# Kernel tuning notes

Measured on AMD Instinct MI355X. Metric: run time of the kernel, lower is better.

## Reference

```python
import jax, jax.numpy as jnp
import numpy as np

NUM_HEADS = 16
D_MODEL = 1024
DEPTH = D_MODEL // NUM_HEADS
B, S = 4, 1024  # q,k seq len = S; v seq len = S-1


def setup_inputs() -> dict:
    key = jax.random.key(0)
    ks = jax.random.split(key, 6)
    scale = 1.0 / np.sqrt(D_MODEL)
    return {
        "v": jax.random.normal(ks[0], (B, S - 1, D_MODEL), dtype=jnp.float32),
        "k": jax.random.normal(ks[1], (B, S, D_MODEL), dtype=jnp.float32),
        "q": jax.random.normal(ks[2], (B, S, D_MODEL), dtype=jnp.float32),
        "mask": jnp.zeros((B, S - 1, S - 1), dtype=jnp.float32),
        "Wv": jax.random.normal(ks[3], (D_MODEL, D_MODEL), dtype=jnp.float32) * scale,
        "bv": jnp.zeros((D_MODEL,), dtype=jnp.float32),
        "Wd": jax.random.normal(ks[4], (D_MODEL, D_MODEL), dtype=jnp.float32) * scale,
        "bd": jnp.zeros((D_MODEL,), dtype=jnp.float32),
    }


def _split_heads(x):
    # (B, T, d_model) -> (B, H, T, depth)
    b, t, _ = x.shape
    return x.reshape(b, t, NUM_HEADS, DEPTH).transpose(0, 2, 1, 3)


def reference(v, k, q, mask, Wv, bv, Wd, bd):
    # 3-D q/k path: qq=q, kk=k (q_layers/k_layers/wq/wk unused)
    vv = v @ Wv + bv                       # (B, S-1, d_model)
    qh = _split_heads(q)                   # (B, H, S, depth)
    kh = _split_heads(k)                   # (B, H, S, depth)
    vh = _split_heads(vv)                  # (B, H, S-1, depth)

    scores = jnp.einsum('bhqd,bhkd->bhqk', qh, kh)      # (B, H, S, S)
    scores = scores[:, :, 1:, :-1]                      # (B, H, S-1, S-1)
    dk = jnp.asarray(DEPTH, scores.dtype)
    nl = jax.nn.relu(scores / jnp.sqrt(dk))
    nl = nl + mask[:, None, :, :] * (-1e9)
    att = jax.nn.softmax(nl, axis=-1)                   # (B, H, S-1, S-1)

    out = jnp.einsum('bhqk,bhkd->bhqd', att, vh)        # (B, H, S-1, depth)
    out = out.transpose(0, 2, 1, 3).reshape(v.shape[0], -1, D_MODEL)  # (B, S-1, d_model)
    output = out @ Wd + bd
    return output, att
```

## Files before the change

### kernel.cpp

```cpp
#include <hip/hip_runtime.h>
#include <hip/hip_bf16.h>

#define NUM_HEADS 16
#define DM 1024
#define DEPTH 64
#define BB 4
#define SS 1024
#define SL 1023
#define M_ROWS (BB*SL)

typedef __attribute__((ext_vector_type(8))) short short8;
typedef __attribute__((ext_vector_type(4))) float floatx4;

__device__ inline unsigned short f2bf(float f) {
  __hip_bfloat16 hb = __float2bfloat16(f);
  return *reinterpret_cast<unsigned short*>(&hb);
}
__device__ inline short8 ld_frag(const unsigned short* p) {
  return *reinterpret_cast<const short8*>(p);
}

template <bool A_BF16, bool OUT_BF16>
__global__ __launch_bounds__(256) void gemm_bias(
    const void* __restrict__ Av, const float* __restrict__ B,
    const float* __restrict__ bias, void* __restrict__ Cv, int M)
{
  __shared__ unsigned short bshT[128][40];
  const int tid = threadIdx.x;
  const int w = tid >> 6, lane = tid & 63, q4 = lane >> 4, l16 = lane & 15;
  const int wm = w >> 1, wn = w & 1;
  const int rb = blockIdx.y * 128 + wm * 64;
  const int cb = blockIdx.x * 128;
  const int wc = wn * 64;

  floatx4 acc[4][4];
  #pragma unroll
  for (int i = 0; i < 4; i++)
    #pragma unroll
    for (int j = 0; j < 4; j++) acc[i][j] = (floatx4){0.f,0.f,0.f,0.f};

  const int sn = tid & 127;
  const int sk = (tid >> 7) * 16;

  for (int k0 = 0; k0 < DM; k0 += 32) {
    __syncthreads();
    {
      const float* bp = B + (size_t)(k0 + sk) * DM + cb + sn;
      unsigned short tmp[16];
      #pragma unroll
      for (int j = 0; j < 16; j++) tmp[j] = f2bf(bp[(size_t)j * DM]);
      *(uint4*)&bshT[sn][sk]     = *(uint4*)&tmp[0];
      *(uint4*)&bshT[sn][sk + 8] = *(uint4*)&tmp[8];
    }
    __syncthreads();

    short8 af[4];
    #pragma unroll
    for (int i = 0; i < 4; i++) {
      int m = rb + i * 16 + l16;
      if (m < M) {
        if (A_BF16) {
          af[i] = ld_frag((const unsigned short*)Av + (size_t)m * DM + k0 + q4 * 8);
        } else {
          const float* ap = (const float*)Av + (size_t)m * DM + k0 + q4 * 8;
          float4 f0 = *(const float4*)ap;
          float4 f1 = *(const float4*)(ap + 4);
          short8 t;
          t[0]=f2bf(f0.x); t[1]=f2bf(f0.y); t[2]=f2bf(f0.z); t[3]=f2bf(f0.w);
          t[4]=f2bf(f1.x); t[5]=f2bf(f1.y); t[6]=f2bf(f1.z); t[7]=f2bf(f1.w);
          af[i] = t;
        }
      } else {
        af[i] = (short8){0,0,0,0,0,0,0,0};
      }
    }
    #pragma unroll
    for (int jn = 0; jn < 4; jn++) {
      short8 bf = ld_frag(&bshT[wc + jn * 16 + l16][q4 * 8]);
      #pragma unroll
      for (int i = 0; i < 4; i++)
        acc[i][jn] = __builtin_amdgcn_mfma_f32_16x16x32_bf16(af[i], bf, acc[i][jn], 0, 0, 0);
    }
  }

  #pragma unroll
  for (int jn = 0; jn < 4; jn++) {
    int col = cb + wc + jn * 16 + l16;
    float bb = bias[col];
    #pragma unroll
    for (int i = 0; i < 4; i++) {
      #pragma unroll
      for (int r = 0; r < 4; r++) {
        int m = rb + i * 16 + q4 * 4 + r;
        if (m < M) {
          float val = acc[i][jn][r] + bb;
          if (OUT_BF16) ((unsigned short*)Cv)[(size_t)m * DM + col] = f2bf(val);
          else          ((float*)Cv)[(size_t)m * DM + col] = val;
        }
      }
    }
  }
}

__global__ __launch_bounds__(256) void attn_kernel(
    const float* __restrict__ Q, const float* __restrict__ Kg,
    const float* __restrict__ Mask, const unsigned short* __restrict__ VV,
    float* __restrict__ Att, unsigned short* __restrict__ Out2)
{
  const int qt = blockIdx.x, h = blockIdx.y, b = blockIdx.z;
  const int tid = threadIdx.x;
  const int w = tid >> 6, lane = tid & 63, q4 = lane >> 4, l16 = lane & 15;
  const int qi0 = qt * 64;
  const int qb = w * 16;

  __shared__ unsigned short qsh[64][72];
  __shared__ unsigned short ksh[64][72];
  __shared__ unsigned short vshT[64][72];
  __shared__ unsigned short psh[4][16][72];

  {
    int qr = tid >> 2, d0 = (tid & 3) * 16;
    int qi = qi0 + qr;
    unsigned short tmp[16];
    if (qi < SL) {
      const float* src = Q + ((size_t)b * SS + qi + 1) * DM + h * DEPTH + d0;
      #pragma unroll
      for (int j = 0; j < 16; j += 4) {
        float4 f = *(const float4*)(src + j);
        tmp[j+0]=f2bf(f.x); tmp[j+1]=f2bf(f.y); tmp[j+2]=f2bf(f.z); tmp[j+3]=f2bf(f.w);
      }
    } else {
      #pragma unroll
      for (int j = 0; j < 16; j++) tmp[j] = 0;
    }
    *(uint4*)&qsh[qr][d0]     = *(uint4*)&tmp[0];
    *(uint4*)&qsh[qr][d0 + 8] = *(uint4*)&tmp[8];
  }

  auto stageK = [&](int kt) {
    int kr = tid >> 2, d0 = (tid & 3) * 16;
    int kj = kt * 64 + kr;
    unsigned short tmp[16];
    if (kj < SL) {
      const float* src = Kg + ((size_t)b * SS + kj) * DM + h * DEPTH + d0;
      #pragma unroll
      for (int j = 0; j < 16; j += 4) {
        float4 f = *(const float4*)(src + j);
        tmp[j+0]=f2bf(f.x); tmp[j+1]=f2bf(f.y); tmp[j+2]=f2bf(f.z); tmp[j+3]=f2bf(f.w);
      }
    } else {
      #pragma unroll
      for (int j = 0; j < 16; j++) tmp[j] = 0;
    }
    *(uint4*)&ksh[kr][d0]     = *(uint4*)&tmp[0];
    *(uint4*)&ksh[kr][d0 + 8] = *(uint4*)&tmp[8];
  };

  auto stageV = [&](int kt) {
    int d = tid & 63, k16 = (tid >> 6) * 16;
    unsigned short tmp[16];
    #pragma unroll
    for (int j = 0; j < 16; j++) {
      int kj = kt * 64 + k16 + j;
      tmp[j] = (kj < SL) ? VV[((size_t)b * SL + kj) * DM + h * DEPTH + d] : (unsigned short)0;
    }
    *(uint4*)&vshT[d][k16]     = *(uint4*)&tmp[0];
    *(uint4*)&vshT[d][k16 + 8] = *(uint4*)&tmp[8];
  };

  __syncthreads();

  float rsv[4] = {0.f, 0.f, 0.f, 0.f};
  for (int kt = 0; kt < 16; kt++) {
    __syncthreads();
    stageK(kt);
    __syncthreads();
    #pragma unroll
    for (int nt = 0; nt < 4; nt++) {
      floatx4 s = (floatx4){0.f,0.f,0.f,0.f};
      s = __builtin_amdgcn_mfma_f32_16x16x32_bf16(
            ld_frag(&qsh[qb + l16][q4*8]), ld_frag(&ksh[nt*16 + l16][q4*8]), s, 0,0,0);
      s = __builtin_amdgcn_mfma_f32_16x16x32_bf16(
            ld_frag(&qsh[qb + l16][32 + q4*8]), ld_frag(&ksh[nt*16 + l16][32 + q4*8]), s, 0,0,0);
      int kj = kt * 64 + nt * 16 + l16;
      bool kv = kj < SL;
      int qi_b = qi0 + qb + q4 * 4;
      const float* mp = Mask + ((size_t)b * SL + qi_b) * SL + kj;
      #pragma unroll
      for (int r = 0; r < 4; r++) {
        int qi = qi_b + r;
        float mval = (kv && qi < SL) ? mp[(size_t)r * SL] : 0.f;
        float sv = fmaxf(s[r] * 0.125f, 0.f) + mval * (-1e9f);
        float p = kv ? __expf(sv) : 0.f;
        rsv[r] += p;
      }
    }
  }
  #pragma unroll
  for (int r = 0; r < 4; r++) {
    #pragma unroll
    for (int off = 1; off < 16; off <<= 1) rsv[r] += __shfl_xor(rsv[r], off, 64);
  }
  float inv[4];
  #pragma unroll
  for (int r = 0; r < 4; r++) inv[r] = 1.f / rsv[r];

  floatx4 oacc[4];
  #pragma unroll
  for (int i = 0; i < 4; i++) oacc[i] = (floatx4){0.f,0.f,0.f,0.f};

  for (int kt = 0; kt < 16; kt++) {
    __syncthreads();
    stageK(kt);
    stageV(kt);
    __syncthreads();
    #pragma unroll
    for (int nt = 0; nt < 4; nt++) {
      floatx4 s = (floatx4){0.f,0.f,0.f,0.f};
      s = __builtin_amdgcn_mfma_f32_16x16x32_bf16(
            ld_frag(&qsh[qb + l16][q4*8]), ld_frag(&ksh[nt*16 + l16][q4*8]), s, 0,0,0);
      s = __builtin_amdgcn_mfma_f32_16x16x32_bf16(
            ld_frag(&qsh[qb + l16][32 + q4*8]), ld_frag(&ksh[nt*16 + l16][32 + q4*8]), s, 0,0,0);
      int kj = kt * 64 + nt * 16 + l16;
      bool kv = kj < SL;
      int qi_b = qi0 + qb + q4 * 4;
      const float* mp = Mask + ((size_t)b * SL + qi_b) * SL + kj;
      #pragma unroll
      for (int r = 0; r < 4; r++) {
        int qi = qi_b + r;
        bool qv = qi < SL;
        float mval = (kv && qv) ? mp[(size_t)r * SL] : 0.f;
        float sv = fmaxf(s[r] * 0.125f, 0.f) + mval * (-1e9f);
        float p = kv ? __expf(sv) : 0.f;
        float pn = p * inv[r];
        if (kv && qv)
          Att[(((size_t)(b * NUM_HEADS + h)) * SL + qi) * SL + kj] = pn;
        psh[w][q4 * 4 + r][nt * 16 + l16] = f2bf(pn);
      }
    }
    short8 pa0 = ld_frag(&psh[w][l16][q4 * 8]);
    short8 pa1 = ld_frag(&psh[w][l16][32 + q4 * 8]);
    #pragma unroll
    for (int nt2 = 0; nt2 < 4; nt2++) {
      oacc[nt2] = __builtin_amdgcn_mfma_f32_16x16x32_bf16(
                    pa0, ld_frag(&vshT[nt2*16 + l16][q4*8]), oacc[nt2], 0,0,0);
      oacc[nt2] = __builtin_amdgcn_mfma_f32_16x16x32_bf16(
                    pa1, ld_frag(&vshT[nt2*16 + l16][32 + q4*8]), oacc[nt2], 0,0,0);
    }
  }

  #pragma unroll
  for (int nt2 = 0; nt2 < 4; nt2++) {
    #pragma unroll
    for (int r = 0; r < 4; r++) {
      int qi = qi0 + qb + q4 * 4 + r;
      if (qi < SL)
        Out2[((size_t)b * SL + qi) * DM + h * DEPTH + nt2 * 16 + l16] = f2bf(oacc[nt2][r]);
    }
  }
}

extern "C" void kernel_launch(void* const* d_in, const int* in_sizes, int n_in,
                              void* d_out, int out_size, void* d_ws, size_t ws_size,
                              hipStream_t stream) {
  const float* v    = (const float*)d_in[0];
  const float* k    = (const float*)d_in[1];
  const float* q    = (const float*)d_in[2];
  const float* mask = (const float*)d_in[3];
  const float* Wv   = (const float*)d_in[4];
  const float* bv   = (const float*)d_in[5];
  const float* Wd   = (const float*)d_in[6];
  const float* bd   = (const float*)d_in[7];

  float* out = (float*)d_out;
  float* att = out + (size_t)M_ROWS * DM;
  unsigned short* vv   = (unsigned short*)d_ws;
  unsigned short* out2 = vv + (size_t)M_ROWS * DM;

  gemm_bias<false, true><<<dim3(DM/128, (M_ROWS+127)/128), 256, 0, stream>>>(
      (const void*)v, Wv, bv, (void*)vv, M_ROWS);
  attn_kernel<<<dim3(16, NUM_HEADS, BB), 256, 0, stream>>>(q, k, mask, vv, att, out2);
  gemm_bias<true, false><<<dim3(DM/128, (M_ROWS+127)/128), 256, 0, stream>>>(
      (const void*)out2, Wd, bd, (void*)out, M_ROWS);
}
```

Before: 778.4 us.

## Cache unnormalized probabilities in LDS and pre-transpose weights to bf16

The attention kernel now computes QK^T once per block instead of twice. It keeps the unnormalized bf16 probabilities for the full key row in a large LDS buffer, writes the normalized attention rows with coalesced stores, and applies the normalization to the PV output at the end. A new prep kernel converts both weight matrices to bf16 and transposes them, so the GEMMs stage A and B tiles into LDS with vector loads instead of strided per-element fp32 loads. The roughly 132KB of LDS per attention block limits occupancy, and the row sums are now taken from bf16-rounded values.

```diff
diff --git a/kernel.cpp b/kernel.cpp
--- a/kernel.cpp
+++ b/kernel.cpp
@@ -8,6 +8,7 @@
 #define SS 1024
 #define SL 1023
 #define M_ROWS (BB*SL)
+#define M_PAD 4096
 
 typedef __attribute__((ext_vector_type(8))) short short8;
 typedef __attribute__((ext_vector_type(4))) float floatx4;
@@ -16,22 +17,49 @@
   __hip_bfloat16 hb = __float2bfloat16(f);
   return *reinterpret_cast<unsigned short*>(&hb);
 }
+__device__ inline float bf2fu(unsigned short u) {
+  union { unsigned int i; float f; } x; x.i = ((unsigned int)u) << 16; return x.f;
+}
 __device__ inline short8 ld_frag(const unsigned short* p) {
   return *reinterpret_cast<const short8*>(p);
 }
 
-template <bool A_BF16, bool OUT_BF16>
+__global__ __launch_bounds__(256) void prep_wt(
+    const float* __restrict__ Wv, const float* __restrict__ Wd,
+    unsigned short* __restrict__ WvT, unsigned short* __restrict__ WdT)
+{
+  const float* W = blockIdx.z ? Wd : Wv;
+  unsigned short* WT = blockIdx.z ? WdT : WvT;
+  __shared__ unsigned short tile[64][66];
+  int n0 = blockIdx.x * 64, k0 = blockIdx.y * 64;
+  int c = threadIdx.x & 63, g = threadIdx.x >> 6;
+  #pragma unroll
+  for (int i = 0; i < 16; i++) {
+    int kk = g * 16 + i;
+    tile[kk][c] = f2bf(W[(size_t)(k0 + kk) * DM + n0 + c]);
+  }
+  __syncthreads();
+  #pragma unroll
+  for (int i = 0; i < 16; i++) {
+    int nn = g * 16 + i;
+    WT[(size_t)(n0 + nn) * DM + k0 + c] = tile[c][nn];
+  }
+}
+
+template <bool A_FP32, bool OUT_BF16>
 __global__ __launch_bounds__(256) void gemm_bias(
-    const void* __restrict__ Av, const float* __restrict__ B,
+    const void* __restrict__ Av, const unsigned short* __restrict__ BT,
     const float* __restrict__ bias, void* __restrict__ Cv, int M)
 {
-  __shared__ unsigned short bshT[128][40];
+  __shared__ unsigned short Ash[128][32];
+  __shared__ unsigned short Bsh[128][32];
   const int tid = threadIdx.x;
   const int w = tid >> 6, lane = tid & 63, q4 = lane >> 4, l16 = lane & 15;
   const int wm = w >> 1, wn = w & 1;
-  const int rb = blockIdx.y * 128 + wm * 64;
+  const int rb = blockIdx.y * 128;
   const int cb = blockIdx.x * 128;
-  const int wc = wn * 64;
+  const int r0 = tid >> 2;
+  const int kc0 = (tid & 3) * 8;
 
   floatx4 acc[4][4];
   #pragma unroll
@@ -39,61 +67,53 @@
     #pragma unroll
     for (int j = 0; j < 4; j++) acc[i][j] = (floatx4){0.f,0.f,0.f,0.f};
 
-  const int sn = tid & 127;
-  const int sk = (tid >> 7) * 16;
+  const int ra0 = min(rb + r0, M - 1);
+  const int ra1 = min(rb + 64 + r0, M - 1);
 
   for (int k0 = 0; k0 < DM; k0 += 32) {
     __syncthreads();
-    {
-      const float* bp = B + (size_t)(k0 + sk) * DM + cb + sn;
-      unsigned short tmp[16];
-      #pragma unroll
-      for (int j = 0; j < 16; j++) tmp[j] = f2bf(bp[(size_t)j * DM]);
-      *(uint4*)&bshT[sn][sk]     = *(uint4*)&tmp[0];
-      *(uint4*)&bshT[sn][sk + 8] = *(uint4*)&tmp[8];
-    }
-    __syncthreads();
-
-    short8 af[4];
+    if (A_FP32) {
+      const float* g0 = (const float*)Av + (size_t)ra0 * DM + k0 + kc0;
+      const float* g1 = (const float*)Av + (size_t)ra1 * DM + k0 + kc0;
+      float4 x0 = *(const float4*)g0, x1 = *(const float4*)(g0 + 4);
+      float4 y0 = *(const float4*)g1, y1 = *(const float4*)(g1 + 4);
+      unsigned short t0[8] = {f2bf(x0.x),f2bf(x0.y),f2bf(x0.z),f2bf(x0.w),
+                              f2bf(x1.x),f2bf(x1.y),f2bf(x1.z),f2bf(x1.w)};
+      unsigned short t1[8] = {f2bf(y0.x),f2bf(y0.y),f2bf(y0.z),f2bf(y0.w),
+                              f2bf(y1.x),f2bf(y1.y),f2bf(y1.z),f2bf(y1.w)};
+      *(uint4*)&Ash[r0][kc0]      = *(uint4*)t0;
+      *(uint4*)&Ash[64 + r0][kc0] = *(uint4*)t1;
+    } else {
+      *(uint4*)&Ash[r0][kc0]      = *(const uint4*)((const unsigned short*)Av + (size_t)ra0 * DM + k0 + kc0);
+      *(uint4*)&Ash[64 + r0][kc0] = *(const uint4*)((const unsigned short*)Av + (size_t)ra1 * DM + k0 + kc0);
+    }
+    *(uint4*)&Bsh[r0][kc0]      = *(const uint4*)(BT + (size_t)(cb + r0) * DM + k0 + kc0);
+    *(uint4*)&Bsh[64 + r0][kc0] = *(const uint4*)(BT + (size_t)(cb + 64 + r0) * DM + k0 + kc0);
+    __syncthreads();
+
+    short8 af[4], bfr[4];
+    #pragma unroll
+    for (int i = 0; i < 4; i++) af[i]  = ld_frag(&Ash[wm*64 + i*16 + l16][q4*8]);
+    #pragma unroll
+    for (int j = 0; j < 4; j++) bfr[j] = ld_frag(&Bsh[wn*64 + j*16 + l16][q4*8]);
+    #pragma unroll
+    for (int j = 0; j < 4; j++)
+      #pragma unroll
+      for (int i = 0; i < 4; i++)
+        acc[i][j] = __builtin_amdgcn_mfma_f32_16x16x32_bf16(af[i], bfr[j], acc[i][j], 0, 0, 0);
+  }
+
+  #pragma unroll
+  for (int j = 0; j < 4; j++) {
+    int col = cb + wn*64 + j*16 + l16;
+    float bb = bias[col];
     #pragma unroll
     for (int i = 0; i < 4; i++) {
-      int m = rb + i * 16 + l16;
-      if (m < M) {
-        if (A_BF16) {
-          af[i] = ld_frag((const unsigned short*)Av + (size_t)m * DM + k0 + q4 * 8);
-        } else {
-          const float* ap = (const float*)Av + (size_t)m * DM + k0 + q4 * 8;
-          float4 f0 = *(const float4*)ap;
-          float4 f1 = *(const float4*)(ap + 4);
-          short8 t;
-          t[0]=f2bf(f0.x); t[1]=f2bf(f0.y); t[2]=f2bf(f0.z); t[3]=f2bf(f0.w);
-          t[4]=f2bf(f1.x); t[5]=f2bf(f1.y); t[6]=f2bf(f1.z); t[7]=f2bf(f1.w);
-          af[i] = t;
-        }
-      } else {
-        af[i] = (short8){0,0,0,0,0,0,0,0};
-      }
-    }
-    #pragma unroll
-    for (int jn = 0; jn < 4; jn++) {
-      short8 bf = ld_frag(&bshT[wc + jn * 16 + l16][q4 * 8]);
-      #pragma unroll
-      for (int i = 0; i < 4; i++)
-        acc[i][jn] = __builtin_amdgcn_mfma_f32_16x16x32_bf16(af[i], bf, acc[i][jn], 0, 0, 0);
-    }
-  }
-
-  #pragma unroll
-  for (int jn = 0; jn < 4; jn++) {
-    int col = cb + wc + jn * 16 + l16;
-    float bb = bias[col];
-    #pragma unroll
-    for (int i = 0; i < 4; i++) {
       #pragma unroll
       for (int r = 0; r < 4; r++) {
-        int m = rb + i * 16 + q4 * 4 + r;
+        int m = rb + wm*64 + i*16 + q4*4 + r;
         if (m < M) {
-          float val = acc[i][jn][r] + bb;
+          float val = acc[i][j][r] + bb;
           if (OUT_BF16) ((unsigned short*)Cv)[(size_t)m * DM + col] = f2bf(val);
           else          ((float*)Cv)[(size_t)m * DM + col] = val;
         }
@@ -113,10 +133,9 @@
   const int qi0 = qt * 64;
   const int qb = w * 16;
 
+  __shared__ unsigned short psh[64][1032];
   __shared__ unsigned short qsh[64][72];
-  __shared__ unsigned short ksh[64][72];
-  __shared__ unsigned short vshT[64][72];
-  __shared__ unsigned short psh[4][16][72];
+  __shared__ unsigned short kvsh[64][72];
 
   {
     int qr = tid >> 2, d0 = (tid & 3) * 16;
@@ -127,7 +146,7 @@
       #pragma unroll
       for (int j = 0; j < 16; j += 4) {
         float4 f = *(const float4*)(src + j);
-        tmp[j+0]=f2bf(f.x); tmp[j+1]=f2bf(f.y); tmp[j+2]=f2bf(f.z); tmp[j+3]=f2bf(f.w);
+        tmp[j]=f2bf(f.x); tmp[j+1]=f2bf(f.y); tmp[j+2]=f2bf(f.z); tmp[j+3]=f2bf(f.w);
       }
     } else {
       #pragma unroll
@@ -136,116 +155,101 @@
     *(uint4*)&qsh[qr][d0]     = *(uint4*)&tmp[0];
     *(uint4*)&qsh[qr][d0 + 8] = *(uint4*)&tmp[8];
   }
-
-  auto stageK = [&](int kt) {
-    int kr = tid >> 2, d0 = (tid & 3) * 16;
-    int kj = kt * 64 + kr;
-    unsigned short tmp[16];
-    if (kj < SL) {
-      const float* src = Kg + ((size_t)b * SS + kj) * DM + h * DEPTH + d0;
-      #pragma unroll
-      for (int j = 0; j < 16; j += 4) {
-        float4 f = *(const float4*)(src + j);
-        tmp[j+0]=f2bf(f.x); tmp[j+1]=f2bf(f.y); tmp[j+2]=f2bf(f.z); tmp[j+3]=f2bf(f.w);
-      }
-    } else {
-      #pragma unroll
-      for (int j = 0; j < 16; j++) tmp[j] = 0;
-    }
-    *(uint4*)&ksh[kr][d0]     = *(uint4*)&tmp[0];
-    *(uint4*)&ksh[kr][d0 + 8] = *(uint4*)&tmp[8];
-  };
-
-  auto stageV = [&](int kt) {
-    int d = tid & 63, k16 = (tid >> 6) * 16;
-    unsigned short tmp[16];
-    #pragma unroll
-    for (int j = 0; j < 16; j++) {
-      int kj = kt * 64 + k16 + j;
-      tmp[j] = (kj < SL) ? VV[((size_t)b * SL + kj) * DM + h * DEPTH + d] : (unsigned short)0;
-    }
-    *(uint4*)&vshT[d][k16]     = *(uint4*)&tmp[0];
-    *(uint4*)&vshT[d][k16 + 8] = *(uint4*)&tmp[8];
-  };
-
   __syncthreads();
+  const short8 qf0 = ld_frag(&qsh[qb + l16][q4*8]);
+  const short8 qf1 = ld_frag(&qsh[qb + l16][32 + q4*8]);
 
   float rsv[4] = {0.f, 0.f, 0.f, 0.f};
+
   for (int kt = 0; kt < 16; kt++) {
     __syncthreads();
-    stageK(kt);
-    __syncthreads();
+    {
+      int kr = tid >> 2, d0 = (tid & 3) * 16;
+      int kj = kt * 64 + kr;
+      unsigned short tmp[16];
+      if (kj < SL) {
+        const float* src = Kg + ((size_t)b * SS + kj) * DM + h * DEPTH + d0;
+        #pragma unroll
+        for (int j = 0; j < 16; j += 4) {
+          float4 f = *(const float4*)(src + j);
+          tmp[j]=f2bf(f.x); tmp[j+1]=f2bf(f.y); tmp[j+2]=f2bf(f.z); tmp[j+3]=f2bf(f.w);
+        }
+      } else {
+        #pragma unroll
+        for (int j = 0; j < 16; j++) tmp[j] = 0;
+      }
+      *(uint4*)&kvsh[kr][d0]     = *(uint4*)&tmp[0];
+      *(uint4*)&kvsh[kr][d0 + 8] = *(uint4*)&tmp[8];
+    }
+    __syncthreads();
+
     #pragma unroll
     for (int nt = 0; nt < 4; nt++) {
       floatx4 s = (floatx4){0.f,0.f,0.f,0.f};
-      s = __builtin_amdgcn_mfma_f32_16x16x32_bf16(
-            ld_frag(&qsh[qb + l16][q4*8]), ld_frag(&ksh[nt*16 + l16][q4*8]), s, 0,0,0);
-      s = __builtin_amdgcn_mfma_f32_16x16x32_bf16(
-            ld_frag(&qsh[qb + l16][32 + q4*8]), ld_frag(&ksh[nt*16 + l16][32 + q4*8]), s, 0,0,0);
+      s = __builtin_amdgcn_mfma_f32_16x16x32_bf16(qf0, ld_frag(&kvsh[nt*16 + l16][q4*8]), s, 0,0,0);
+      s = __builtin_amdgcn_mfma_f32_16x16x32_bf16(qf1, ld_frag(&kvsh[nt*16 + l16][32 + q4*8]), s, 0,0,0);
       int kj = kt * 64 + nt * 16 + l16;
       bool kv = kj < SL;
       int qi_b = qi0 + qb + q4 * 4;
       const float* mp = Mask + ((size_t)b * SL + qi_b) * SL + kj;
       #pragma unroll
       for (int r = 0; r < 4; r++) {
-        int qi = qi_b + r;
-        float mval = (kv && qi < SL) ? mp[(size_t)r * SL] : 0.f;
-        float sv = fmaxf(s[r] * 0.125f, 0.f) + mval * (-1e9f);
-        float p = kv ? __expf(sv) : 0.f;
-        rsv[r] += p;
-      }
-    }
-  }
-  #pragma unroll
-  for (int r = 0; r < 4; r++) {
-    #pragma unroll
-    for (int off = 1; off < 16; off <<= 1) rsv[r] += __shfl_xor(rsv[r], off, 64);
-  }
-  float inv[4];
-  #pragma unroll
-  for (int r = 0; r < 4; r++) inv[r] = 1.f / rsv[r];
-
-  floatx4 oacc[4];
-  #pragma unroll
-  for (int i = 0; i < 4; i++) oacc[i] = (floatx4){0.f,0.f,0.f,0.f};
-
-  for (int kt = 0; kt < 16; kt++) {
-    __syncthreads();
-    stageK(kt);
-    stageV(kt);
-    __syncthreads();
-    #pragma unroll
-    for (int nt = 0; nt < 4; nt++) {
-      floatx4 s = (floatx4){0.f,0.f,0.f,0.f};
-      s = __builtin_amdgcn_mfma_f32_16x16x32_bf16(
-            ld_frag(&qsh[qb + l16][q4*8]), ld_frag(&ksh[nt*16 + l16][q4*8]), s, 0,0,0);
-      s = __builtin_amdgcn_mfma_f32_16x16x32_bf16(
-            ld_frag(&qsh[qb + l16][32 + q4*8]), ld_frag(&ksh[nt*16 + l16][32 + q4*8]), s, 0,0,0);
-      int kj = kt * 64 + nt * 16 + l16;
-      bool kv = kj < SL;
-      int qi_b = qi0 + qb + q4 * 4;
-      const float* mp = Mask + ((size_t)b * SL + qi_b) * SL + kj;
-      #pragma unroll
-      for (int r = 0; r < 4; r++) {
-        int qi = qi_b + r;
-        bool qv = qi < SL;
+        bool qv = (qi_b + r) < SL;
         float mval = (kv && qv) ? mp[(size_t)r * SL] : 0.f;
         float sv = fmaxf(s[r] * 0.125f, 0.f) + mval * (-1e9f);
         float p = kv ? __expf(sv) : 0.f;
-        float pn = p * inv[r];
-        if (kv && qv)
-          Att[(((size_t)(b * NUM_HEADS + h)) * SL + qi) * SL + kj] = pn;
-        psh[w][q4 * 4 + r][nt * 16 + l16] = f2bf(pn);
-      }
-    }
-    short8 pa0 = ld_frag(&psh[w][l16][q4 * 8]);
-    short8 pa1 = ld_frag(&psh[w][l16][32 + q4 * 8]);
+        unsigned short u = f2bf(p);
+        psh[qb + q4*4 + r][kt*64 + nt*16 + l16] = u;
+        rsv[r] += bf2fu(u);
+      }
+    }
+  }
+
+  float inv4[4];
+  #pragma unroll
+  for (int r = 0; r < 4; r++) {
+    float s = rsv[r];
+    s += __shfl_xor(s, 1, 64); s += __shfl_xor(s, 2, 64);
+    s += __shfl_xor(s, 4, 64); s += __shfl_xor(s, 8, 64);
+    inv4[r] = 1.f / s;
+  }
+
+  #pragma unroll
+  for (int rr = 0; rr < 16; rr++) {
+    int row = qb + rr;
+    int qi = qi0 + row;
+    if (qi < SL) {
+      float iv = __shfl(inv4[rr & 3], (rr >> 2) * 16, 64);
+      float* arow = Att + (((size_t)(b * NUM_HEADS + h)) * SL + qi) * SL;
+      for (int col = lane; col < SL; col += 64)
+        arow[col] = bf2fu(psh[row][col]) * iv;
+    }
+  }
+
+  floatx4 oacc[4];
+  #pragma unroll
+  for (int i = 0; i < 4; i++) oacc[i] = (floatx4){0.f,0.f,0.f,0.f};
+
+  for (int kt = 0; kt < 16; kt++) {
+    __syncthreads();
+    {
+      int d = tid & 63, k16 = (tid >> 6) * 16;
+      unsigned short tmp[16];
+      #pragma unroll
+      for (int j = 0; j < 16; j++) {
+        int kj = kt * 64 + k16 + j;
+        tmp[j] = (kj < SL) ? VV[((size_t)b * SL + kj) * DM + h * DEPTH + d] : (unsigned short)0;
+      }
+      *(uint4*)&kvsh[d][k16]     = *(uint4*)&tmp[0];
+      *(uint4*)&kvsh[d][k16 + 8] = *(uint4*)&tmp[8];
+    }
+    __syncthreads();
+    short8 pa0 = ld_frag(&psh[qb + l16][kt*64 + q4*8]);
+    short8 pa1 = ld_frag(&psh[qb + l16][kt*64 + 32 + q4*8]);
     #pragma unroll
     for (int nt2 = 0; nt2 < 4; nt2++) {
-      oacc[nt2] = __builtin_amdgcn_mfma_f32_16x16x32_bf16(
-                    pa0, ld_frag(&vshT[nt2*16 + l16][q4*8]), oacc[nt2], 0,0,0);
-      oacc[nt2] = __builtin_amdgcn_mfma_f32_16x16x32_bf16(
-                    pa1, ld_frag(&vshT[nt2*16 + l16][32 + q4*8]), oacc[nt2], 0,0,0);
+      oacc[nt2] = __builtin_amdgcn_mfma_f32_16x16x32_bf16(pa0, ld_frag(&kvsh[nt2*16 + l16][q4*8]), oacc[nt2], 0,0,0);
+      oacc[nt2] = __builtin_amdgcn_mfma_f32_16x16x32_bf16(pa1, ld_frag(&kvsh[nt2*16 + l16][32 + q4*8]), oacc[nt2], 0,0,0);
     }
   }
 
@@ -253,9 +257,9 @@
   for (int nt2 = 0; nt2 < 4; nt2++) {
     #pragma unroll
     for (int r = 0; r < 4; r++) {
-      int qi = qi0 + qb + q4 * 4 + r;
+      int qi = qi0 + qb + q4*4 + r;
       if (qi < SL)
-        Out2[((size_t)b * SL + qi) * DM + h * DEPTH + nt2 * 16 + l16] = f2bf(oacc[nt2][r]);
+        Out2[((size_t)b * SL + qi) * DM + h * DEPTH + nt2*16 + l16] = f2bf(oacc[nt2][r] * inv4[r]);
     }
   }
 }
@@ -274,12 +278,16 @@
 
   float* out = (float*)d_out;
   float* att = out + (size_t)M_ROWS * DM;
+
   unsigned short* vv   = (unsigned short*)d_ws;
-  unsigned short* out2 = vv + (size_t)M_ROWS * DM;
-
-  gemm_bias<false, true><<<dim3(DM/128, (M_ROWS+127)/128), 256, 0, stream>>>(
-      (const void*)v, Wv, bv, (void*)vv, M_ROWS);
+  unsigned short* out2 = vv + (size_t)M_PAD * DM;
+  unsigned short* WvT  = out2 + (size_t)M_PAD * DM;
+  unsigned short* WdT  = WvT + (size_t)DM * DM;
+
+  prep_wt<<<dim3(DM/64, DM/64, 2), 256, 0, stream>>>(Wv, Wd, WvT, WdT);
+  gemm_bias<true, true><<<dim3(DM/128, M_PAD/128), 256, 0, stream>>>(
+      (const void*)v, WvT, bv, (void*)vv, M_ROWS);
   attn_kernel<<<dim3(16, NUM_HEADS, BB), 256, 0, stream>>>(q, k, mask, vv, att, out2);
-  gemm_bias<true, false><<<dim3(DM/128, (M_ROWS+127)/128), 256, 0, stream>>>(
-      (const void*)out2, Wd, bd, (void*)out, M_ROWS);
-}
+  gemm_bias<false, false><<<dim3(DM/128, M_PAD/128), 256, 0, stream>>>(
+      (const void*)out2, WdT, bd, (void*)out, M_ROWS);
+}
```

Measured after the change: 898.5 us. +15.4%, slower.
